# Optimization experiments

Hardware: AMD Instinct MI355X
Metric: run time of the kernel (lower is better)

## Reference

```python
import jax, jax.numpy as jnp
import numpy as np

N = 10000   # nodes
E = 320000  # directed edges (self-loops added inside reference, per PyG default)
H1, C = 4, 128  # gat1: 4 heads x 128; gat2: 1 head x 128
NEG_SLOPE = 0.2


def _glorot(k, shape):
    lim = float(np.sqrt(6.0 / (shape[0] + shape[-1])))
    return jax.random.uniform(k, shape, jnp.float32, -lim, lim)


def setup_inputs() -> dict:
    key = jax.random.key(0)
    ks = jax.random.split(key, 12)
    x = jax.random.normal(ks[0], (N, 2), jnp.float32)
    edge_index = jax.random.randint(ks[1], (2, E), 0, N, dtype=jnp.int32).astype(jnp.int64)
    W1 = _glorot(ks[2], (2, H1 * C))
    att_src1 = _glorot(ks[3], (H1, C))
    att_dst1 = _glorot(ks[4], (H1, C))
    b1 = jnp.zeros((H1 * C,), jnp.float32)
    W2 = _glorot(ks[5], (H1 * C, C))
    att_src2 = _glorot(ks[6], (1, C))
    att_dst2 = _glorot(ks[7], (1, C))
    b2 = jnp.zeros((C,), jnp.float32)
    Wp = _glorot(ks[8], (C, 1))
    bp = jnp.zeros((1,), jnp.float32)
    return dict(x=x, edge_index=edge_index, W1=W1, att_src1=att_src1, att_dst1=att_dst1,
                b1=b1, W2=W2, att_src2=att_src2, att_dst2=att_dst2, b2=b2, Wp=Wp, bp=bp)


def _gat_conv(x, src, dst, W, a_src, a_dst, b, heads, ch, concat):
    n = x.shape[0]
    h = (x @ W).reshape(n, heads, ch)                         # [N,H,C]
    # per-node attention halves, gathered per edge
    e = jax.nn.leaky_relu((h * a_src).sum(-1)[src] + (h * a_dst).sum(-1)[dst],
                          NEG_SLOPE)                           # [E,H]
    # segment softmax over incoming edges of each destination node
    m = jax.ops.segment_max(e, dst, num_segments=n)            # [N,H]
    p = jnp.exp(e - m[dst])
    s = jax.ops.segment_sum(p, dst, num_segments=n)
    alpha = p / (s[dst] + 1e-16)                               # [E,H]
    out = jax.ops.segment_sum(h[src] * alpha[..., None], dst, num_segments=n)  # [N,H,C]
    out = out.reshape(n, heads * ch) if concat else out.mean(axis=1)
    return out + b


def reference(x, edge_index, W1, att_src1, att_dst1, b1, W2, att_src2, att_dst2, b2, Wp, bp):
    n = x.shape[0]
    loop = jnp.arange(n, dtype=edge_index.dtype)               # PyG add_self_loops=True
    src = jnp.concatenate([edge_index[0], loop])
    dst = jnp.concatenate([edge_index[1], loop])
    h = jax.nn.relu(_gat_conv(x, src, dst, W1, att_src1, att_dst1, b1, H1, C, True))
    h = jax.nn.relu(_gat_conv(h, src, dst, W2, att_src2, att_dst2, b2, 1, C, True))
    logits = h @ Wp + bp                                       # [N,1]
    return logits.squeeze(-1)
```

## Files before the change

kernel.cpp:

```cpp
#include <hip/hip_runtime.h>
#include <hip/hip_fp16.h>
#include <math.h>

#define N_NODES 10000
#define E_IN    320000
#define E_TOT   330000
#define H1      4
#define C       128
#define F1      512

typedef _Float16 f16x8 __attribute__((ext_vector_type(8)));
typedef float    f32x4 __attribute__((ext_vector_type(4)));

__global__ __launch_bounds__(256) void k_as1z(
    const float* __restrict__ x, const float* __restrict__ W1,
    const float* __restrict__ asw, const float* __restrict__ adw,
    float4* __restrict__ as1v, float4* __restrict__ ad1v, int* __restrict__ deg)
{
    __shared__ float red[4][8];
    __shared__ float prep_s[16];
    int tid = threadIdx.x;
    {
        int j = tid;
        int j2 = tid + 256;
        float w0a = W1[j],  w1a = W1[F1 + j];
        float w0b = W1[j2], w1b = W1[F1 + j2];
        float aa = asw[j], dd = adw[j], ab = asw[j2], db = adw[j2];
        float q0 = w0a*aa, q1 = w1a*aa, q2 = w0a*dd, q3 = w1a*dd;
        float q4 = w0b*ab, q5 = w1b*ab, q6 = w0b*db, q7 = w1b*db;
        #pragma unroll
        for (int o = 32; o > 0; o >>= 1) {
            q0 += __shfl_down(q0, o); q1 += __shfl_down(q1, o);
            q2 += __shfl_down(q2, o); q3 += __shfl_down(q3, o);
            q4 += __shfl_down(q4, o); q5 += __shfl_down(q5, o);
            q6 += __shfl_down(q6, o); q7 += __shfl_down(q7, o);
        }
        int wave = tid >> 6, lane = tid & 63;
        if (lane == 0) {
            red[wave][0] = q0; red[wave][1] = q1; red[wave][2] = q2; red[wave][3] = q3;
            red[wave][4] = q4; red[wave][5] = q5; red[wave][6] = q6; red[wave][7] = q7;
        }
        __syncthreads();
        if (tid < 16) {
            int t = tid >> 2;
            int h = tid & 3;
            int w0 = (h & 1) * 2;
            int r  = t + (h >> 1) * 4;
            prep_s[t*4 + h] = red[w0][r] + red[w0+1][r];
        }
        __syncthreads();
    }
    int n = blockIdx.x * 256 + tid;
    if (n >= N_NODES) return;
    deg[n] = 0;
    float x0 = x[2*n], x1 = x[2*n+1];
    float4 A0 = *(const float4*)(prep_s);
    float4 A1 = *(const float4*)(prep_s + 4);
    float4 D0 = *(const float4*)(prep_s + 8);
    float4 D1 = *(const float4*)(prep_s + 12);
    as1v[n] = make_float4(x0*A0.x + x1*A1.x, x0*A0.y + x1*A1.y,
                          x0*A0.z + x1*A1.z, x0*A0.w + x1*A1.w);
    ad1v[n] = make_float4(x0*D0.x + x1*D1.x, x0*D0.y + x1*D1.y,
                          x0*D0.z + x1*D1.z, x0*D0.w + x1*D1.w);
}

__global__ void k_hist(const int* __restrict__ dsti, int* __restrict__ deg) {
    int t = blockIdx.x * blockDim.x + threadIdx.x;
    if (t >= E_TOT) return;
    int d = (t < E_IN) ? dsti[t] : (t - E_IN);
    atomicAdd(&deg[d], 1);
}

__global__ __launch_bounds__(256) void k_scan(
    const int* __restrict__ deg, int* __restrict__ offs, int* __restrict__ cursor)
{
    __shared__ int part[256];
    int tid = threadIdx.x;
    const int CH = (N_NODES + 255) / 256;
    int start = tid * CH;
    int sum = 0;
    for (int i = 0; i < CH; ++i) { int idx = start + i; if (idx < N_NODES) sum += deg[idx]; }
    part[tid] = sum;
    __syncthreads();
    for (int off = 1; off < 256; off <<= 1) {
        int v = (tid >= off) ? part[tid - off] : 0;
        __syncthreads();
        part[tid] += v;
        __syncthreads();
    }
    int base = (tid == 0) ? 0 : part[tid - 1];
    for (int i = 0; i < CH; ++i) {
        int idx = start + i;
        if (idx < N_NODES) { offs[idx] = base; cursor[idx] = base; base += deg[idx]; }
    }
    if (tid == 255) offs[N_NODES] = base;
}

__global__ void k_scatter(const int* __restrict__ srci, const int* __restrict__ dsti,
                          int* __restrict__ cursor, int* __restrict__ scsr) {
    int t = blockIdx.x * blockDim.x + threadIdx.x;
    if (t >= E_TOT) return;
    int d = (t < E_IN) ? dsti[t] : (t - E_IN);
    int s = (t < E_IN) ? srci[t] : (t - E_IN);
    int pos = atomicAdd(&cursor[d], 1);
    scsr[pos] = s;
}

__global__ __launch_bounds__(256) void k_fused1(
    const int* __restrict__ offs, const int* __restrict__ scsr,
    const float4* __restrict__ as1v, const float4* __restrict__ ad1v,
    const float2* __restrict__ xv, float* __restrict__ wxn)
{
    int node = blockIdx.x * 16 + (threadIdx.x >> 4);
    int sub = threadIdx.x & 15;
    int beg = offs[node], end = offs[node + 1];
    float4 ad = ad1v[node];
    float s0 = 0.f, s1 = 0.f, s2 = 0.f, s3 = 0.f;
    float w00 = 0.f, w01 = 0.f, w10 = 0.f, w11 = 0.f;
    float w20 = 0.f, w21 = 0.f, w30 = 0.f, w31 = 0.f;
    for (int i = beg + sub; i < end; i += 16) {
        int s = scsr[i];
        float4 a = as1v[s];
        float2 xs = xv[s];
        float e0 = a.x + ad.x; e0 = e0 > 0.f ? e0 : 0.2f*e0;
        float e1 = a.y + ad.y; e1 = e1 > 0.f ? e1 : 0.2f*e1;
        float e2 = a.z + ad.z; e2 = e2 > 0.f ? e2 : 0.2f*e2;
        float e3 = a.w + ad.w; e3 = e3 > 0.f ? e3 : 0.2f*e3;
        float p0 = __expf(e0), p1 = __expf(e1), p2 = __expf(e2), p3 = __expf(e3);
        s0 += p0; s1 += p1; s2 += p2; s3 += p3;
        w00 += p0*xs.x; w01 += p0*xs.y; w10 += p1*xs.x; w11 += p1*xs.y;
        w20 += p2*xs.x; w21 += p2*xs.y; w30 += p3*xs.x; w31 += p3*xs.y;
    }
    #pragma unroll
    for (int o = 1; o < 16; o <<= 1) {
        s0 += __shfl_xor(s0, o); s1 += __shfl_xor(s1, o);
        s2 += __shfl_xor(s2, o); s3 += __shfl_xor(s3, o);
        w00 += __shfl_xor(w00, o); w01 += __shfl_xor(w01, o);
        w10 += __shfl_xor(w10, o); w11 += __shfl_xor(w11, o);
        w20 += __shfl_xor(w20, o); w21 += __shfl_xor(w21, o);
        w30 += __shfl_xor(w30, o); w31 += __shfl_xor(w31, o);
    }
    if (sub == 0) {
        float i0 = 1.f/(s0 + 1e-16f), i1 = 1.f/(s1 + 1e-16f);
        float i2 = 1.f/(s2 + 1e-16f), i3 = 1.f/(s3 + 1e-16f);
        float4* W = (float4*)(wxn + node*8);
        W[0] = make_float4(w00*i0, w01*i0, w10*i1, w11*i1);
        W[1] = make_float4(w20*i2, w21*i2, w30*i3, w31*i3);
    }
}

__global__ __launch_bounds__(256, 1) void k_gemm2(
    const float* __restrict__ wxn, const float* __restrict__ W1,
    const float* __restrict__ b1, const float* __restrict__ W2,
    const float* __restrict__ asw, const float* __restrict__ adw,
    __half* __restrict__ h2h, float* __restrict__ as2, float* __restrict__ ad2)
{
    __shared__ _Float16 w2t[F1 * C];
    int tid = threadIdx.x;
    {
        int c0 = (tid & 63) * 2;
        int kh = tid >> 6;
        int xr0 = (c0 & 7) << 3;
        int xr1 = ((c0 + 1) & 7) << 3;
        for (int kb = 0; kb < 128; kb += 8) {
            int k0 = kh * 128 + kb;
            f16x8 p0, p1;
            #pragma unroll
            for (int jj = 0; jj < 8; ++jj) {
                float2 w = *(const float2*)(W2 + (k0 + jj) * C + c0);
                p0[jj] = (_Float16)w.x;
                p1[jj] = (_Float16)w.y;
            }
            *(f16x8*)(&w2t[c0 * F1 + (k0 ^ xr0)])       = p0;
            *(f16x8*)(&w2t[(c0 + 1) * F1 + (k0 ^ xr1)]) = p1;
        }
    }
    __syncthreads();

    int wid = tid >> 6, lane = tid & 63;
    int tile = blockIdx.x * 4 + wid;
    if (tile >= N_NODES / 16) return;
    int n0w = tile * 16;
    int col = lane & 15;
    int krow = (lane >> 4) * 8;
    int qr4 = (lane >> 4) * 4;
    int node = n0w + col;

    float4 wv0 = *(const float4*)(wxn + node * 8);
    float4 wv1 = *(const float4*)(wxn + node * 8 + 4);

    f32x4 acc[8];
    #pragma unroll
    for (int mt = 0; mt < 8; ++mt) acc[mt] = (f32x4){0.f, 0.f, 0.f, 0.f};

    int xr = (col & 7) << 3;
    const float* W1r0 = W1;
    const float* W1r1 = W1 + F1;

    #pragma unroll
    for (int h = 0; h < 4; ++h) {
        float wa = (h == 0) ? wv0.x : (h == 1) ? wv0.z : (h == 2) ? wv1.x : wv1.z;
        float wb = (h == 0) ? wv0.y : (h == 1) ? wv0.w : (h == 2) ? wv1.y : wv1.w;
        #pragma unroll
        for (int kq = 0; kq < 4; ++kq) {
            int kc = h * 4 + kq;
            int k0 = kc * 32 + krow;
            float4 a0 = *(const float4*)(W1r0 + k0);
            float4 a1 = *(const float4*)(W1r0 + k0 + 4);
            float4 c0 = *(const float4*)(W1r1 + k0);
            float4 c1 = *(const float4*)(W1r1 + k0 + 4);
            float4 b0 = *(const float4*)(b1 + k0);
            float4 b1v = *(const float4*)(b1 + k0 + 4);
            f16x8 bf;
            float v;
            v = wa*a0.x + wb*c0.x + b0.x;  bf[0] = (_Float16)(v > 0.f ? v : 0.f);
            v = wa*a0.y + wb*c0.y + b0.y;  bf[1] = (_Float16)(v > 0.f ? v : 0.f);
            v = wa*a0.z + wb*c0.z + b0.z;  bf[2] = (_Float16)(v > 0.f ? v : 0.f);
            v = wa*a0.w + wb*c0.w + b0.w;  bf[3] = (_Float16)(v > 0.f ? v : 0.f);
            v = wa*a1.x + wb*c1.x + b1v.x; bf[4] = (_Float16)(v > 0.f ? v : 0.f);
            v = wa*a1.y + wb*c1.y + b1v.y; bf[5] = (_Float16)(v > 0.f ? v : 0.f);
            v = wa*a1.z + wb*c1.z + b1v.z; bf[6] = (_Float16)(v > 0.f ? v : 0.f);
            v = wa*a1.w + wb*c1.w + b1v.w; bf[7] = (_Float16)(v > 0.f ? v : 0.f);
            int kbase = col * F1 + (k0 ^ xr);
            #pragma unroll
            for (int mt = 0; mt < 8; ++mt) {
                f16x8 af = *(const f16x8*)(&w2t[mt * 16 * F1 + kbase]);
                acc[mt] = __builtin_amdgcn_mfma_f32_16x16x32_f16(af, bf, acc[mt], 0, 0, 0);
            }
        }
    }

    float ps = 0.f, pd = 0.f;
    __half* hbase = h2h + (size_t)node * C + qr4;
    #pragma unroll
    for (int mt = 0; mt < 8; ++mt) {
        f32x4 a = acc[mt];
        __half2 lo = __floats2half2_rn(a[0], a[1]);
        __half2 hi = __floats2half2_rn(a[2], a[3]);
        uint2 u; u.x = *(uint*)&lo; u.y = *(uint*)&hi;
        *(uint2*)(hbase + mt * 16) = u;
        float4 av = *(const float4*)(asw + mt * 16 + qr4);
        float4 dv = *(const float4*)(adw + mt * 16 + qr4);
        ps += a[0]*av.x + a[1]*av.y + a[2]*av.z + a[3]*av.w;
        pd += a[0]*dv.x + a[1]*dv.y + a[2]*dv.z + a[3]*dv.w;
    }
    ps += __shfl_xor(ps, 16); ps += __shfl_xor(ps, 32);
    pd += __shfl_xor(pd, 16); pd += __shfl_xor(pd, 32);
    if (lane < 16) { as2[n0w + lane] = ps; ad2[n0w + lane] = pd; }
}

__global__ __launch_bounds__(256) void k_agg2(
    const int* __restrict__ offs, const int* __restrict__ scsr,
    const float* __restrict__ as2, const float* __restrict__ ad2,
    const __half* __restrict__ h2h, const float* __restrict__ b2,
    const float* __restrict__ Wp, const float* __restrict__ bp,
    float* __restrict__ out)
{
    int n = blockIdx.x * 4 + (threadIdx.x >> 6);
    int lane = threadIdx.x & 63;
    int beg = offs[n], end = offs[n + 1];
    float adn = ad2[n];
    float accx = 0.f, accy = 0.f, psum = 0.f;
    int i = beg;
    for (; i + 4 <= end; i += 4) {
        int s0 = scsr[i+0], s1 = scsr[i+1], s2 = scsr[i+2], s3 = scsr[i+3];
        float e0 = as2[s0] + adn, e1 = as2[s1] + adn;
        float e2 = as2[s2] + adn, e3 = as2[s3] + adn;
        __half2 q0 = *(const __half2*)(h2h + (size_t)s0*C + 2*lane);
        __half2 q1 = *(const __half2*)(h2h + (size_t)s1*C + 2*lane);
        __half2 q2 = *(const __half2*)(h2h + (size_t)s2*C + 2*lane);
        __half2 q3 = *(const __half2*)(h2h + (size_t)s3*C + 2*lane);
        e0 = e0 > 0.f ? e0 : 0.2f*e0;  float p0 = __expf(e0);
        e1 = e1 > 0.f ? e1 : 0.2f*e1;  float p1 = __expf(e1);
        e2 = e2 > 0.f ? e2 : 0.2f*e2;  float p2 = __expf(e2);
        e3 = e3 > 0.f ? e3 : 0.2f*e3;  float p3 = __expf(e3);
        psum += (p0 + p1) + (p2 + p3);
        float2 f0 = __half22float2(q0), f1 = __half22float2(q1);
        float2 f2 = __half22float2(q2), f3 = __half22float2(q3);
        accx += p0*f0.x + p1*f1.x + p2*f2.x + p3*f3.x;
        accy += p0*f0.y + p1*f1.y + p2*f2.y + p3*f3.y;
    }
    for (; i < end; ++i) {
        int s = scsr[i];
        float e = as2[s] + adn; e = e > 0.f ? e : 0.2f*e;
        float p = __expf(e);
        psum += p;
        __half2 q = *(const __half2*)(h2h + (size_t)s*C + 2*lane);
        float2 f = __half22float2(q);
        accx += p * f.x; accy += p * f.y;
    }
    float inv = 1.f / (psum + 1e-16f);
    float2 bb = *(const float2*)(b2 + 2*lane);
    float2 wp = *(const float2*)(Wp + 2*lane);
    float v0 = accx*inv + bb.x; v0 = v0 > 0.f ? v0 : 0.f;
    float v1 = accy*inv + bb.y; v1 = v1 > 0.f ? v1 : 0.f;
    float contrib = v0*wp.x + v1*wp.y;
    #pragma unroll
    for (int o = 1; o < 64; o <<= 1) contrib += __shfl_xor(contrib, o);
    if (lane == 0) out[n] = contrib + bp[0];
}

extern "C" void kernel_launch(void* const* d_in, const int* in_sizes, int n_in,
                              void* d_out, int out_size, void* d_ws, size_t ws_size,
                              hipStream_t stream)
{
    const float* x    = (const float*)d_in[0];
    const int*   ei   = (const int*)d_in[1];
    const int*   srci = ei;
    const int*   dsti = ei + E_IN;
    const float* W1   = (const float*)d_in[2];
    const float* as1w = (const float*)d_in[3];
    const float* ad1w = (const float*)d_in[4];
    const float* b1   = (const float*)d_in[5];
    const float* W2   = (const float*)d_in[6];
    const float* as2w = (const float*)d_in[7];
    const float* ad2w = (const float*)d_in[8];
    const float* b2   = (const float*)d_in[9];
    const float* Wp   = (const float*)d_in[10];
    const float* bp   = (const float*)d_in[11];
    float* out = (float*)d_out;

    char* ws = (char*)d_ws;
    size_t off = 0;
    auto alloc = [&](size_t bytes) -> char* {
        char* p = ws + off;
        off = (off + bytes + 255) & ~(size_t)255;
        return p;
    };
    float4* as1v   = (float4*)alloc((size_t)N_NODES * 16);
    float4* ad1v   = (float4*)alloc((size_t)N_NODES * 16);
    float*  wxn    = (float*)alloc((size_t)N_NODES * 8 * 4);
    __half* h2h    = (__half*)alloc((size_t)N_NODES * C * 2);
    float*  as2    = (float*)alloc((size_t)N_NODES * 4);
    float*  ad2    = (float*)alloc((size_t)N_NODES * 4);
    int*    deg    = (int*)alloc((size_t)N_NODES * 4);
    int*    offs   = (int*)alloc((size_t)(N_NODES + 1) * 4);
    int*    cursor = (int*)alloc((size_t)N_NODES * 4);
    int*    scsr   = (int*)alloc((size_t)E_TOT * 4);

    const int EB = 256;
    const int egrid = (E_TOT + EB - 1) / EB;
    const int ngrid = (N_NODES + 255) / 256;

    k_as1z<<<ngrid, 256, 0, stream>>>(x, W1, as1w, ad1w, as1v, ad1v, deg);
    k_hist<<<egrid, EB, 0, stream>>>(dsti, deg);
    k_scan<<<1, 256, 0, stream>>>(deg, offs, cursor);
    k_scatter<<<egrid, EB, 0, stream>>>(srci, dsti, cursor, scsr);
    k_fused1<<<N_NODES / 16, 256, 0, stream>>>(offs, scsr, as1v, ad1v,
                                               (const float2*)x, wxn);
    k_gemm2<<<(N_NODES/16 + 3) / 4, 256, 0, stream>>>(wxn, W1, b1, W2, as2w, ad2w,
                                                      h2h, as2, ad2);
    k_agg2<<<N_NODES / 4, 256, 0, stream>>>(offs, scsr, as2, ad2, h2h, b2, Wp, bp, out);
}
```

Before: 188.8 us.

## Precompute swizzled fp16 W2, prefetch CSR indices, split agg2 edges across half-waves

```diff
diff --git a/kernel.cpp b/kernel.cpp
--- a/kernel.cpp
+++ b/kernel.cpp
@@ -64,6 +64,23 @@
                           x0*D0.z + x1*D1.z, x0*D0.w + x1*D1.w);
 }
 
+__global__ __launch_bounds__(256) void k_w2cvt(
+    const float* __restrict__ W2, _Float16* __restrict__ w2h)
+{
+    int t = blockIdx.x * 256 + threadIdx.x;
+    int e0 = t * 4;
+    int c = e0 >> 9;
+    int kk0 = e0 & 511;
+    int xr = (c & 7) << 3;
+    _Float16 o[4];
+    #pragma unroll
+    for (int j = 0; j < 4; ++j) {
+        int k = (kk0 + j) ^ xr;
+        o[j] = (_Float16)W2[k * C + c];
+    }
+    *(uint2*)(w2h + c * F1 + kk0) = *(uint2*)o;
+}
+
 __global__ void k_hist(const int* __restrict__ dsti, int* __restrict__ deg) {
     int t = blockIdx.x * blockDim.x + threadIdx.x;
     if (t >= E_TOT) return;
@@ -118,18 +135,27 @@
     float s0 = 0.f, s1 = 0.f, s2 = 0.f, s3 = 0.f;
     float w00 = 0.f, w01 = 0.f, w10 = 0.f, w11 = 0.f;
     float w20 = 0.f, w21 = 0.f, w30 = 0.f, w31 = 0.f;
-    for (int i = beg + sub; i < end; i += 16) {
+    int i = beg + sub;
+    if (i < end) {
         int s = scsr[i];
-        float4 a = as1v[s];
-        float2 xs = xv[s];
-        float e0 = a.x + ad.x; e0 = e0 > 0.f ? e0 : 0.2f*e0;
-        float e1 = a.y + ad.y; e1 = e1 > 0.f ? e1 : 0.2f*e1;
-        float e2 = a.z + ad.z; e2 = e2 > 0.f ? e2 : 0.2f*e2;
-        float e3 = a.w + ad.w; e3 = e3 > 0.f ? e3 : 0.2f*e3;
-        float p0 = __expf(e0), p1 = __expf(e1), p2 = __expf(e2), p3 = __expf(e3);
-        s0 += p0; s1 += p1; s2 += p2; s3 += p3;
-        w00 += p0*xs.x; w01 += p0*xs.y; w10 += p1*xs.x; w11 += p1*xs.y;
-        w20 += p2*xs.x; w21 += p2*xs.y; w30 += p3*xs.x; w31 += p3*xs.y;
+        for (;;) {
+            float4 a = as1v[s];
+            float2 xs = xv[s];
+            int inext = i + 16;
+            bool more = inext < end;
+            int snext = 0;
+            if (more) snext = scsr[inext];
+            float e0 = a.x + ad.x; e0 = e0 > 0.f ? e0 : 0.2f*e0;
+            float e1 = a.y + ad.y; e1 = e1 > 0.f ? e1 : 0.2f*e1;
+            float e2 = a.z + ad.z; e2 = e2 > 0.f ? e2 : 0.2f*e2;
+            float e3 = a.w + ad.w; e3 = e3 > 0.f ? e3 : 0.2f*e3;
+            float p0 = __expf(e0), p1 = __expf(e1), p2 = __expf(e2), p3 = __expf(e3);
+            s0 += p0; s1 += p1; s2 += p2; s3 += p3;
+            w00 += p0*xs.x; w01 += p0*xs.y; w10 += p1*xs.x; w11 += p1*xs.y;
+            w20 += p2*xs.x; w21 += p2*xs.y; w30 += p3*xs.x; w31 += p3*xs.y;
+            if (!more) break;
+            i = inext; s = snext;
+        }
     }
     #pragma unroll
     for (int o = 1; o < 16; o <<= 1) {
@@ -151,29 +177,16 @@
 
 __global__ __launch_bounds__(256, 1) void k_gemm2(
     const float* __restrict__ wxn, const float* __restrict__ W1,
-    const float* __restrict__ b1, const float* __restrict__ W2,
+    const float* __restrict__ b1, const _Float16* __restrict__ w2h,
     const float* __restrict__ asw, const float* __restrict__ adw,
     __half* __restrict__ h2h, float* __restrict__ as2, float* __restrict__ ad2)
 {
     __shared__ _Float16 w2t[F1 * C];
     int tid = threadIdx.x;
-    {
-        int c0 = (tid & 63) * 2;
-        int kh = tid >> 6;
-        int xr0 = (c0 & 7) << 3;
-        int xr1 = ((c0 + 1) & 7) << 3;
-        for (int kb = 0; kb < 128; kb += 8) {
-            int k0 = kh * 128 + kb;
-            f16x8 p0, p1;
-            #pragma unroll
-            for (int jj = 0; jj < 8; ++jj) {
-                float2 w = *(const float2*)(W2 + (k0 + jj) * C + c0);
-                p0[jj] = (_Float16)w.x;
-                p1[jj] = (_Float16)w.y;
-            }
-            *(f16x8*)(&w2t[c0 * F1 + (k0 ^ xr0)])       = p0;
-            *(f16x8*)(&w2t[(c0 + 1) * F1 + (k0 ^ xr1)]) = p1;
-        }
+    #pragma unroll
+    for (int it = 0; it < 32; ++it) {
+        int idx = (it * 256 + tid) * 8;
+        *(f16x8*)(w2t + idx) = *(const f16x8*)(w2h + idx);
     }
     __syncthreads();
 
@@ -258,45 +271,56 @@
 {
     int n = blockIdx.x * 4 + (threadIdx.x >> 6);
     int lane = threadIdx.x & 63;
+    int half = lane >> 5;
+    int cl = lane & 31;
     int beg = offs[n], end = offs[n + 1];
     float adn = ad2[n];
-    float accx = 0.f, accy = 0.f, psum = 0.f;
-    int i = beg;
-    for (; i + 4 <= end; i += 4) {
-        int s0 = scsr[i+0], s1 = scsr[i+1], s2 = scsr[i+2], s3 = scsr[i+3];
+    float a0 = 0.f, a1 = 0.f, a2 = 0.f, a3 = 0.f, psum = 0.f;
+    int i = beg + half;
+    for (; i + 6 < end; i += 8) {
+        int s0 = scsr[i], s1 = scsr[i+2], s2 = scsr[i+4], s3 = scsr[i+6];
         float e0 = as2[s0] + adn, e1 = as2[s1] + adn;
         float e2 = as2[s2] + adn, e3 = as2[s3] + adn;
-        __half2 q0 = *(const __half2*)(h2h + (size_t)s0*C + 2*lane);
-        __half2 q1 = *(const __half2*)(h2h + (size_t)s1*C + 2*lane);
-        __half2 q2 = *(const __half2*)(h2h + (size_t)s2*C + 2*lane);
-        __half2 q3 = *(const __half2*)(h2h + (size_t)s3*C + 2*lane);
+        uint2 q0 = *(const uint2*)(h2h + (size_t)s0*C + 4*cl);
+        uint2 q1 = *(const uint2*)(h2h + (size_t)s1*C + 4*cl);
+        uint2 q2 = *(const uint2*)(h2h + (size_t)s2*C + 4*cl);
+        uint2 q3 = *(const uint2*)(h2h + (size_t)s3*C + 4*cl);
         e0 = e0 > 0.f ? e0 : 0.2f*e0;  float p0 = __expf(e0);
         e1 = e1 > 0.f ? e1 : 0.2f*e1;  float p1 = __expf(e1);
         e2 = e2 > 0.f ? e2 : 0.2f*e2;  float p2 = __expf(e2);
         e3 = e3 > 0.f ? e3 : 0.2f*e3;  float p3 = __expf(e3);
         psum += (p0 + p1) + (p2 + p3);
-        float2 f0 = __half22float2(q0), f1 = __half22float2(q1);
-        float2 f2 = __half22float2(q2), f3 = __half22float2(q3);
-        accx += p0*f0.x + p1*f1.x + p2*f2.x + p3*f3.x;
-        accy += p0*f0.y + p1*f1.y + p2*f2.y + p3*f3.y;
-    }
-    for (; i < end; ++i) {
+        float2 f0a = __half22float2(*(__half2*)&q0.x), f0b = __half22float2(*(__half2*)&q0.y);
+        float2 f1a = __half22float2(*(__half2*)&q1.x), f1b = __half22float2(*(__half2*)&q1.y);
+        float2 f2a = __half22float2(*(__half2*)&q2.x), f2b = __half22float2(*(__half2*)&q2.y);
+        float2 f3a = __half22float2(*(__half2*)&q3.x), f3b = __half22float2(*(__half2*)&q3.y);
+        a0 += p0*f0a.x + p1*f1a.x + p2*f2a.x + p3*f3a.x;
+        a1 += p0*f0a.y + p1*f1a.y + p2*f2a.y + p3*f3a.y;
+        a2 += p0*f0b.x + p1*f1b.x + p2*f2b.x + p3*f3b.x;
+        a3 += p0*f0b.y + p1*f1b.y + p2*f2b.y + p3*f3b.y;
+    }
+    for (; i < end; i += 2) {
         int s = scsr[i];
         float e = as2[s] + adn; e = e > 0.f ? e : 0.2f*e;
         float p = __expf(e);
         psum += p;
-        __half2 q = *(const __half2*)(h2h + (size_t)s*C + 2*lane);
-        float2 f = __half22float2(q);
-        accx += p * f.x; accy += p * f.y;
-    }
+        uint2 q = *(const uint2*)(h2h + (size_t)s*C + 4*cl);
+        float2 fa = __half22float2(*(__half2*)&q.x), fb = __half22float2(*(__half2*)&q.y);
+        a0 += p*fa.x; a1 += p*fa.y; a2 += p*fb.x; a3 += p*fb.y;
+    }
+    a0 += __shfl_xor(a0, 32); a1 += __shfl_xor(a1, 32);
+    a2 += __shfl_xor(a2, 32); a3 += __shfl_xor(a3, 32);
+    psum += __shfl_xor(psum, 32);
     float inv = 1.f / (psum + 1e-16f);
-    float2 bb = *(const float2*)(b2 + 2*lane);
-    float2 wp = *(const float2*)(Wp + 2*lane);
-    float v0 = accx*inv + bb.x; v0 = v0 > 0.f ? v0 : 0.f;
-    float v1 = accy*inv + bb.y; v1 = v1 > 0.f ? v1 : 0.f;
-    float contrib = v0*wp.x + v1*wp.y;
-    #pragma unroll
-    for (int o = 1; o < 64; o <<= 1) contrib += __shfl_xor(contrib, o);
+    float4 bb = *(const float4*)(b2 + 4*cl);
+    float4 wp = *(const float4*)(Wp + 4*cl);
+    float v0 = a0*inv + bb.x; v0 = v0 > 0.f ? v0 : 0.f;
+    float v1 = a1*inv + bb.y; v1 = v1 > 0.f ? v1 : 0.f;
+    float v2 = a2*inv + bb.z; v2 = v2 > 0.f ? v2 : 0.f;
+    float v3 = a3*inv + bb.w; v3 = v3 > 0.f ? v3 : 0.f;
+    float contrib = v0*wp.x + v1*wp.y + v2*wp.z + v3*wp.w;
+    #pragma unroll
+    for (int o = 1; o < 32; o <<= 1) contrib += __shfl_xor(contrib, o);
     if (lane == 0) out[n] = contrib + bp[0];
 }
 
@@ -327,28 +351,30 @@
         off = (off + bytes + 255) & ~(size_t)255;
         return p;
     };
-    float4* as1v   = (float4*)alloc((size_t)N_NODES * 16);
-    float4* ad1v   = (float4*)alloc((size_t)N_NODES * 16);
-    float*  wxn    = (float*)alloc((size_t)N_NODES * 8 * 4);
-    __half* h2h    = (__half*)alloc((size_t)N_NODES * C * 2);
-    float*  as2    = (float*)alloc((size_t)N_NODES * 4);
-    float*  ad2    = (float*)alloc((size_t)N_NODES * 4);
-    int*    deg    = (int*)alloc((size_t)N_NODES * 4);
-    int*    offs   = (int*)alloc((size_t)(N_NODES + 1) * 4);
-    int*    cursor = (int*)alloc((size_t)N_NODES * 4);
-    int*    scsr   = (int*)alloc((size_t)E_TOT * 4);
+    float4*    as1v   = (float4*)alloc((size_t)N_NODES * 16);
+    float4*    ad1v   = (float4*)alloc((size_t)N_NODES * 16);
+    float*     wxn    = (float*)alloc((size_t)N_NODES * 8 * 4);
+    __half*    h2h    = (__half*)alloc((size_t)N_NODES * C * 2);
+    _Float16*  w2h    = (_Float16*)alloc((size_t)F1 * C * 2);
+    float*     as2    = (float*)alloc((size_t)N_NODES * 4);
+    float*     ad2    = (float*)alloc((size_t)N_NODES * 4);
+    int*       deg    = (int*)alloc((size_t)N_NODES * 4);
+    int*       offs   = (int*)alloc((size_t)(N_NODES + 1) * 4);
+    int*       cursor = (int*)alloc((size_t)N_NODES * 4);
+    int*       scsr   = (int*)alloc((size_t)E_TOT * 4);
 
     const int EB = 256;
     const int egrid = (E_TOT + EB - 1) / EB;
     const int ngrid = (N_NODES + 255) / 256;
 
     k_as1z<<<ngrid, 256, 0, stream>>>(x, W1, as1w, ad1w, as1v, ad1v, deg);
+    k_w2cvt<<<64, 256, 0, stream>>>(W2, w2h);
     k_hist<<<egrid, EB, 0, stream>>>(dsti, deg);
     k_scan<<<1, 256, 0, stream>>>(deg, offs, cursor);
     k_scatter<<<egrid, EB, 0, stream>>>(srci, dsti, cursor, scsr);
     k_fused1<<<N_NODES / 16, 256, 0, stream>>>(offs, scsr, as1v, ad1v,
                                                (const float2*)x, wxn);
-    k_gemm2<<<(N_NODES/16 + 3) / 4, 256, 0, stream>>>(wxn, W1, b1, W2, as2w, ad2w,
+    k_gemm2<<<(N_NODES/16 + 3) / 4, 256, 0, stream>>>(wxn, W1, b1, w2h, as2w, ad2w,
                                                       h2h, as2, ad2);
     k_agg2<<<N_NODES / 4, 256, 0, stream>>>(offs, scsr, as2, ad2, h2h, b2, Wp, bp, out);
 }
```

Result: no change. 185.8 us (-1.6%).
